# Kernel optimization log

Measured on AMD Instinct MI355X. Metric: run time of the kernel, lower is better.

The kernel has to match this reference:

```python
import jax, jax.numpy as jnp
import numpy as np

TEMP = 0.07
GAMMA1 = 0.8
GAMMA2 = 0.8
TAU = 0.1
BETA = 40.0
NUM_CT = 5
EPS = float(np.finfo(np.float32).eps)


def setup_inputs() -> dict:
    key = jax.random.key(0)
    ks = jax.random.split(key, 12)
    B, D, N, Bc = 8192, 512, 1000000, 4096
    img = jax.random.normal(ks[0], (B, D), jnp.float32)
    txt = jax.random.normal(ks[1], (B, D), jnp.float32)
    # CLIP-style unit-norm features keep sim in [-1,1] so exp() stays stable
    img = img / jnp.linalg.norm(img, axis=1, keepdims=True)
    txt = txt / jnp.linalg.norm(txt, axis=1, keepdims=True)
    image_ids = jax.random.randint(ks[2], (B,), 0, N)
    text_ids = jax.random.randint(ks[3], (B,), 0, N)
    slabel = jax.random.randint(ks[4], (B,), 0, 2)
    img_feas_c = jax.random.normal(ks[5], (Bc, D), jnp.float32)
    img_feas_c = img_feas_c / jnp.linalg.norm(img_feas_c, axis=1, keepdims=True)
    txt_feas_c = jax.random.normal(ks[6], (NUM_CT, D), jnp.float32)
    txt_feas_c = txt_feas_c / jnp.linalg.norm(txt_feas_c, axis=1, keepdims=True)
    labels_c = jax.random.randint(ks[7], (Bc,), 0, NUM_CT)
    last_loss_c = jax.random.uniform(ks[8], (Bc,), jnp.float32) * 2.0
    # persistent moving-average buffers (positive values, as they hold past exp-means)
    s_I = jax.random.uniform(ks[9], (N,), jnp.float32) + 0.5
    s_T = jax.random.uniform(ks[10], (N,), jnp.float32) + 0.5
    u = jnp.zeros((NUM_CT,), jnp.float32)
    return dict(image_features=img, text_features=txt, image_ids=image_ids,
                text_ids=text_ids, slabel=slabel, epoch=1,
                img_feas_c=img_feas_c, txt_feas_c=txt_feas_c, labels_c=labels_c,
                last_loss_c=last_loss_c, s_I=s_I, s_T=s_T, u=u)


def reference(image_features, text_features, image_ids, text_ids, slabel, epoch,
              img_feas_c, txt_feas_c, labels_c, last_loss_c, s_I, s_T, u):
    sg = jax.lax.stop_gradient
    # pairwise similarity GEMM  [B, B]
    sim = jnp.einsum('id,jd->ij', image_features, text_features)
    diag = jnp.diagonal(sim)
    pos = slabel == 1
    neg = ~pos
    pos_image_ids = image_ids[pos]
    pos_text_ids = text_ids[pos]
    # masked pairwise similarity differences: [P, B-P] and [B-P, P]
    image_diffs = (sim - diag[:, None])[pos][:, neg]
    text_diffs = (sim - diag[None, :])[neg][:, pos]
    image_diffs_d = sg(image_diffs / TEMP)
    text_diffs_d = sg(text_diffs / TEMP)
    exp_i = jnp.exp(image_diffs_d)
    exp_t = jnp.exp(text_diffs_d)
    g_I = jnp.mean(exp_i, axis=1, keepdims=True)   # [P, 1]
    g_T = jnp.mean(exp_t, axis=0, keepdims=True)   # [1, P]
    if epoch == 0:
        sI = g_I
        sT = g_T
    else:
        sI = ((1.0 - GAMMA1) * s_I[pos_image_ids] + GAMMA1 * g_I.squeeze()).reshape(g_I.shape)
        sT = ((1.0 - GAMMA1) * s_T[pos_text_ids] + GAMMA1 * g_T.squeeze()).reshape(g_T.shape)
    # persistent buffer scatter updates
    s_I_new = s_I.at[pos_image_ids].set(sI.squeeze())
    s_T_new = s_T.at[pos_text_ids].set(sT.squeeze())
    w_i = exp_i / (sI + EPS)
    w_t = exp_t / (sT + EPS)
    image_loss = jnp.mean(w_i * image_diffs, axis=1)
    text_loss = jnp.mean(w_t * text_diffs, axis=0)
    contrastive_loss = image_loss.mean() + text_loss.mean()
    # per-class CE penalty branch
    logits = (1.0 / TAU) * img_feas_c @ txt_feas_c.T           # [Bc, NUM_CT]
    logp = jax.nn.log_softmax(logits, axis=-1)
    ce = -logp[jnp.arange(logits.shape[0]), labels_c]          # [Bc]
    counts = jax.ops.segment_sum(jnp.ones_like(ce), labels_c, num_segments=NUM_CT)
    present = counts > 0
    safe_counts = jnp.maximum(counts, 1.0)
    mean_by_cls = jax.ops.segment_sum(ce, labels_c, num_segments=NUM_CT) / safe_counts
    mean_by_cls_last = jax.ops.segment_sum(last_loss_c, labels_c, num_segments=NUM_CT) / safe_counts
    cv = mean_by_cls - mean_by_cls_last
    u_sum = jnp.sum(jnp.where(present, u, 0.0))
    u_upd = jnp.where(u_sum == 0.0, sg(cv), (1.0 - GAMMA2) * u + GAMMA2 * sg(cv))
    u_new = jnp.where(present, u_upd, u)
    beta = BETA  # cosine=False
    cl = sg(jnp.maximum(beta * u_new, 0.0)) * mean_by_cls * TAU
    n_present = jnp.sum(present.astype(jnp.float32))
    constraint_mean = jnp.sum(jnp.where(present, cl, 0.0)) / n_present
    loss = contrastive_loss + constraint_mean
    return loss, s_I_new, s_T_new, u_new
```

## Files before the change

### kernel.cpp

```cpp
#include <hip/hip_runtime.h>

#define NBATCH 8192
#define DD 512
#define NIDS 1000000
#define BCNT 4096
#define NCT 5
#define INV_TEMP 14.285714285714286f
#define EPSF 1.1920929e-07f
#define FPSCALE 16.0f
#define INV_SIMSCALE (1.0f / 256.0f)

typedef __attribute__((ext_vector_type(4))) float f32x4;
typedef __attribute__((ext_vector_type(2))) long lx2;

#define OFF_LP     ((size_t)0)
#define OFF_CE1    ((size_t)1024)
#define OFF_CE2    ((size_t)2304)
#define OFF_CE3    ((size_t)3584)
#define OFF_POS    ((size_t)(32*1024))
#define OFF_RNK    ((size_t)(64*1024))
#define OFF_CNT    ((size_t)(96*1024))
#define OFF_DA     ((size_t)(100*1024))
#define OFF_RA0    ((size_t)(132*1024))
#define OFF_RB0    ((size_t)(164*1024))
#define OFF_RA1    ((size_t)(196*1024))
#define OFF_RB1    ((size_t)(228*1024))
#define OFF_SIV    ((size_t)(260*1024))
#define OFF_STV    ((size_t)(292*1024))
#define OFF_WINI   ((size_t)(324*1024))
#define OFF_WINT   (OFF_WINI + 4000000)
#define OFF_MA     (OFF_WINT + 4000000)
#define MATB       ((size_t)(8192*512*2))
#define OFF_MB     (OFF_MA + MATB)
#define OFF_MC     (OFF_MB + MATB)
#define OFF_MD     (OFF_MC + MATB)


__global__ __launch_bounds__(256) void k_pre(
        const float* __restrict__ sI, const float* __restrict__ sT,
        float* __restrict__ out,
        float* __restrict__ rA0, float* __restrict__ rB0,
        float* __restrict__ rA1, float* __restrict__ rB1,
        const int* __restrict__ slabel, int* __restrict__ pos,
        int* __restrict__ rnk, int* __restrict__ cnts,
        const float* __restrict__ imgc, const float* __restrict__ tfc,
        const int* __restrict__ labels, const float* __restrict__ lastl,
        float* __restrict__ ce1, float* __restrict__ ce2, float* __restrict__ ce3) {
    int bid = blockIdx.x;
    int tid = threadIdx.x;
    int iv = bid * 256 + tid;
    if (iv < NIDS) {
        out[1 + iv] = sI[iv];
        out[1 + NIDS + iv] = sT[iv];
    }
    if (iv < NBATCH) { rA0[iv] = 0.f; rB0[iv] = 0.f; rA1[iv] = 0.f; rB1[iv] = 0.f; }
    if (bid > 64) return;

    if (bid == 64) {
        __shared__ int sums[256];
        int base = tid * 32;
        int c = 0;
        for (int j = 0; j < 32; ++j) c += (slabel[base + j] == 1);
        sums[tid] = c;
        __syncthreads();
        for (int off = 1; off < 256; off <<= 1) {
            int add = (tid >= off) ? sums[tid - off] : 0;
            __syncthreads();
            sums[tid] += add;
            __syncthreads();
        }
        int p = sums[tid] - c;
        for (int j = 0; j < 32; ++j) {
            int idx = base + j;
            if (slabel[idx] == 1) { pos[p] = idx; rnk[idx] = p; p++; }
            else rnk[idx] = idx - p;
        }
        if (tid == 255) { cnts[0] = sums[255]; cnts[1] = NBATCH - sums[255]; }
    } else {
        int cb = bid;
        __shared__ float tS[NCT * DD];
        __shared__ float sce[NCT], scn[NCT], sls[NCT];
        for (int j = tid; j < NCT * DD; j += 256) tS[j] = tfc[j];
        if (tid < NCT) { sce[tid] = 0.f; scn[tid] = 0.f; sls[tid] = 0.f; }
        __syncthreads();
        int lane = tid & 63;
        int wid = tid >> 6;
        for (int it = 0; it < 16; ++it) {
            int r = it * 256 + cb * 4 + wid;
            const float4* ip = (const float4*)(imgc + (size_t)r * DD) + lane * 2;
            float4 a0 = ip[0], a1 = ip[1];
            float p[NCT];
#pragma unroll
            for (int c = 0; c < NCT; ++c) {
                const float* t = &tS[c * DD + lane * 8];
                p[c] = a0.x * t[0] + a0.y * t[1] + a0.z * t[2] + a0.w * t[3]
                     + a1.x * t[4] + a1.y * t[5] + a1.z * t[6] + a1.w * t[7];
            }
#pragma unroll
            for (int c = 0; c < NCT; ++c)
                for (int off = 32; off; off >>= 1) p[c] += __shfl_xor(p[c], off);
            if (lane == 0) {
                float l[NCT];
                float mx = -1e30f;
#pragma unroll
                for (int c = 0; c < NCT; ++c) { l[c] = p[c] * 10.0f; mx = fmaxf(mx, l[c]); }
                float ssum = 0.f;
#pragma unroll
                for (int c = 0; c < NCT; ++c) ssum += __expf(l[c] - mx);
                float lse = mx + __logf(ssum);
                int lb = labels[r];
                float ce = lse - l[lb];
                atomicAdd(&sce[lb], ce);
                atomicAdd(&scn[lb], 1.f);
                atomicAdd(&sls[lb], lastl[r]);
            }
        }
        __syncthreads();
        if (tid < NCT) {
            ce1[cb * 5 + tid] = sce[tid];
            ce2[cb * 5 + tid] = scn[tid];
            ce3[cb * 5 + tid] = sls[tid];
        }
    }
}

__global__ __launch_bounds__(256) void k_gather(
        const float* __restrict__ img, const float* __restrict__ txt,
        const int* __restrict__ slabel, const int* __restrict__ rnk,
        const int* __restrict__ image_ids, const int* __restrict__ text_ids,
        int* __restrict__ winI, int* __restrict__ winT,
        unsigned char* __restrict__ mA, unsigned char* __restrict__ mB,
        unsigned char* __restrict__ mC, unsigned char* __restrict__ mD,
        float* __restrict__ dA) {
    int tid = threadIdx.x;
    int kk = blockIdx.x * 256 + tid;
    if (kk < NBATCH) {
        winI[image_ids[kk]] = -1;
        winT[text_ids[kk]] = -1;
    }
    int i = blockIdx.x * 4 + (tid >> 6);
    int g = tid & 63;
    const float4* ip = (const float4*)(img + (size_t)i * DD) + g * 2;
    const float4* tp = (const float4*)(txt + (size_t)i * DD) + g * 2;
    float4 v0 = ip[0], v1 = ip[1], t0 = tp[0], t1 = tp[1];
    float part = v0.x * t0.x + v0.y * t0.y + v0.z * t0.z + v0.w * t0.w
               + v1.x * t1.x + v1.y * t1.y + v1.z * t1.z + v1.w * t1.w;
    for (int off = 32; off; off >>= 1) part += __shfl_xor(part, off);

    int lab = (slabel[i] == 1);
    int r = rnk[i];

    int ilo = __builtin_amdgcn_cvt_pk_fp8_f32(v0.x * FPSCALE, v0.y * FPSCALE, 0, 0);
    ilo = __builtin_amdgcn_cvt_pk_fp8_f32(v0.z * FPSCALE, v0.w * FPSCALE, ilo, 1);
    int ihi = __builtin_amdgcn_cvt_pk_fp8_f32(v1.x * FPSCALE, v1.y * FPSCALE, 0, 0);
    ihi = __builtin_amdgcn_cvt_pk_fp8_f32(v1.z * FPSCALE, v1.w * FPSCALE, ihi, 1);
    int tlo = __builtin_amdgcn_cvt_pk_fp8_f32(t0.x * FPSCALE, t0.y * FPSCALE, 0, 0);
    tlo = __builtin_amdgcn_cvt_pk_fp8_f32(t0.z * FPSCALE, t0.w * FPSCALE, tlo, 1);
    int thi = __builtin_amdgcn_cvt_pk_fp8_f32(t1.x * FPSCALE, t1.y * FPSCALE, 0, 0);
    thi = __builtin_amdgcn_cvt_pk_fp8_f32(t1.z * FPSCALE, t1.w * FPSCALE, thi, 1);

    int rl = r & 127;
    int cp = g & 7;
    int gran = cp & 3, half = cp >> 2;
    int swb = ((gran * 16) ^ ((rl & 6) << 3)) + half * 8;
    size_t off = (size_t)(r >> 7) * 65536 + (size_t)(g >> 3) * 8192 + rl * 64 + swb;
    unsigned char* dI = lab ? mA : mD;
    unsigned char* dT = lab ? mC : mB;
    *(int2*)(dI + off) = make_int2(ilo, ihi);
    *(int2*)(dT + off) = make_int2(tlo, thi);
    if (lab && g == 0) dA[r] = part;
}

__device__ __forceinline__ void gl16(const void* src, void* lds) {
    __builtin_amdgcn_global_load_lds((const __attribute__((address_space(1))) void*)src,
                                     (__attribute__((address_space(3))) void*)lds, 16, 0, 0);
}

#define VM4()  asm volatile("s_waitcnt vmcnt(4)" ::: "memory")
#define VM0()  asm volatile("s_waitcnt vmcnt(0)" ::: "memory")
#define BARR() asm volatile("s_barrier" ::: "memory")

__global__ __launch_bounds__(256) void k_gemm(
        const unsigned char* __restrict__ mA, const unsigned char* __restrict__ mB,
        const unsigned char* __restrict__ mC, const unsigned char* __restrict__ mD,
        const float* __restrict__ dA, const int* __restrict__ cnts,
        float* __restrict__ rA0, float* __restrict__ rB0,
        float* __restrict__ rA1, float* __restrict__ rB1) {
    int P = cnts[0], Nn = cnts[1];
    int bm = blockIdx.x * 128, bn = blockIdx.y * 128;
    if (bm >= P || bn >= Nn) return;
    int z = blockIdx.z;
    const unsigned char* Ap = (z ? mC : mA) + (size_t)blockIdx.x * 65536;
    const unsigned char* Bp = (z ? mD : mB) + (size_t)blockIdx.y * 65536;
    float* rA = z ? rA1 : rA0;
    float* rB = z ? rB1 : rB0;

    __shared__ __align__(16) char SRAW[36864];
    char* S = SRAW;

    int tid = threadIdx.x;
    int lane = tid & 63;
    int wid = tid >> 6;
    int wr = wid >> 1, wc = wid & 1;
    int bo = tid * 16;

    int kswz = ((lane >> 4) * 16) ^ ((lane & 6) << 3);
    int abyte = (wr * 64 + (lane & 15)) * 64 + kswz;
    int bbyte = (wc * 64 + (lane & 15)) * 64 + kswz;

    f32x4 acc[4][4];
#pragma unroll
    for (int m = 0; m < 4; ++m)
#pragma unroll
        for (int n = 0; n < 4; ++n) acc[m][n] = (f32x4){0.f, 0.f, 0.f, 0.f};

#define STAGE(kt, p) do { \
        gl16(Ap + (kt) * 8192 + bo,        S + (p) * 16384 + bo); \
        gl16(Ap + (kt) * 8192 + bo + 4096, S + (p) * 16384 + bo + 4096); \
        gl16(Bp + (kt) * 8192 + bo,        S + (p) * 16384 + 8192 + bo); \
        gl16(Bp + (kt) * 8192 + bo + 4096, S + (p) * 16384 + 8192 + bo + 4096); } while (0)

    STAGE(0, 0);
    STAGE(1, 1);
    VM4();
    BARR();

#pragma unroll
    for (int kt = 0; kt < 8; ++kt) {
        const int cur = kt & 1;
        const char* base = S + cur * 16384;
        lx2 af[4], bf[4];
#pragma unroll
        for (int m = 0; m < 4; ++m)
            af[m] = *(const lx2*)(base + abyte + m * 1024);
#pragma unroll
        for (int n = 0; n < 4; ++n)
            bf[n] = *(const lx2*)(base + 8192 + bbyte + n * 1024);
#pragma unroll
        for (int m = 0; m < 4; ++m)
#pragma unroll
            for (int n = 0; n < 4; ++n)
                acc[m][n] = __builtin_amdgcn_mfma_f32_16x16x32_fp8_fp8(af[m][0], bf[n][0], acc[m][n], 0, 0, 0);
#pragma unroll
        for (int m = 0; m < 4; ++m)
#pragma unroll
            for (int n = 0; n < 4; ++n)
                acc[m][n] = __builtin_amdgcn_mfma_f32_16x16x32_fp8_fp8(af[m][1], bf[n][1], acc[m][n], 0, 0, 0);
        if (kt < 7) {
            BARR();
            if (kt + 2 < 8) {
                STAGE(kt + 2, cur);
                VM4();
            } else {
                VM0();
            }
            BARR();
        }
    }
#undef STAGE

    BARR();
    float* F = (float*)SRAW;
    int col = lane & 15;
    int rsub = (lane >> 4) * 4;
    int rowbase = bm + wr * 64;
    int colb = bn + wc * 64 + col;
    int fb = ((wc << 7) + (wr << 6)) * 36 + col * 2;
#pragma unroll
    for (int m = 0; m < 4; ++m) {
#pragma unroll
        for (int r = 0; r < 4; ++r) {
            int wrow = m * 16 + rsub + r;
            float dv = dA[rowbase + wrow];
            float pa = 0.f, pb = 0.f;
#pragma unroll
            for (int n = 0; n < 4; ++n) {
                int gcol = colb + n * 16;
                float sv = acc[m][n][r] * INV_SIMSCALE;
                float df = sv - dv;
                float e = (gcol < Nn) ? __expf(df * INV_TEMP) : 0.f;
                pa += e;
                pb += e * df;
            }
            *(float2*)&F[fb + wrow * 36] = make_float2(pa, pb);
        }
    }
    BARR();
    {
        int row = tid >> 1;
        int half = tid & 1;
        const float4* Fr = (const float4*)&F[((half << 7) + row) * 36];
        float sa = 0.f, sb = 0.f;
#pragma unroll
        for (int q = 0; q < 8; ++q) {
            float4 v = Fr[q];
            sa += v.x + v.z;
            sb += v.y + v.w;
        }
        sa += __shfl_xor(sa, 1);
        sb += __shfl_xor(sb, 1);
        int grow = bm + row;
        if (!half && grow < P) {
            atomicAdd(&rA[grow], sa);
            atomicAdd(&rB[grow], sb);
        }
    }
}

__global__ void k_posfin(const int* __restrict__ cnts, const int* __restrict__ pos,
                         const float* __restrict__ rA0, const float* __restrict__ rB0,
                         const float* __restrict__ rA1, const float* __restrict__ rB1,
                         const int* __restrict__ image_ids, const int* __restrict__ text_ids,
                         const float* __restrict__ sIin, const float* __restrict__ sTin,
                         const int* __restrict__ epochp,
                         float* __restrict__ sIv, float* __restrict__ sTv,
                         int* __restrict__ winI, int* __restrict__ winT,
                         float* __restrict__ lp) {
    int k = blockIdx.x * 256 + threadIdx.x;
    int P = cnts[0], Nn = cnts[1];
    float invNn = 1.f / (float)Nn;
    int epoch = epochp[0];
    float lI = 0.f, lT = 0.f;
    if (k < P) {
        int i = pos[k];
        int idI = image_ids[i], idT = text_ids[i];
        float gI = rA0[k] * invNn;
        float sIvk = (epoch == 0) ? gI : 0.2f * sIin[idI] + 0.8f * gI;
        lI = (rB0[k] * invNn) / (sIvk + EPSF);
        float gT = rA1[k] * invNn;
        float sTvk = (epoch == 0) ? gT : 0.2f * sTin[idT] + 0.8f * gT;
        lT = (rB1[k] * invNn) / (sTvk + EPSF);
        sIv[k] = sIvk;
        sTv[k] = sTvk;
        atomicMax(&winI[idI], k);
        atomicMax(&winT[idT], k);
    }
    for (int off = 32; off; off >>= 1) { lI += __shfl_xor(lI, off); lT += __shfl_xor(lT, off); }
    if ((threadIdx.x & 63) == 0) {
        int slot = blockIdx.x * 4 + (threadIdx.x >> 6);
        lp[slot * 2] = lI;
        lp[slot * 2 + 1] = lT;
    }
}

__global__ void k_fin(const int* __restrict__ cnts, const int* __restrict__ pos,
                      const int* __restrict__ image_ids, const int* __restrict__ text_ids,
                      const int* __restrict__ winI, const int* __restrict__ winT,
                      const float* __restrict__ sIv, const float* __restrict__ sTv,
                      const float* __restrict__ lp, const float* __restrict__ ce1,
                      const float* __restrict__ ce2, const float* __restrict__ ce3,
                      const float* __restrict__ u, float* __restrict__ out) {
    int P = cnts[0];
    int k = blockIdx.x * 256 + threadIdx.x;
    if (k < P) {
        int i = pos[k];
        int a = image_ids[i];
        if (winI[a] == k) out[1 + a] = sIv[k];
        int b = text_ids[i];
        if (winT[b] == k) out[1 + NIDS + b] = sTv[k];
    }
    if (blockIdx.x == 0 && threadIdx.x < 64) {
        int lane = threadIdx.x;
        float lI = lp[2 * lane] + lp[2 * (lane + 64)];
        float lT = lp[2 * lane + 1] + lp[2 * (lane + 64) + 1];
        for (int off = 32; off; off >>= 1) { lI += __shfl_xor(lI, off); lT += __shfl_xor(lT, off); }
        float ce[NCT], cn[NCT], ls[NCT];
#pragma unroll
        for (int c = 0; c < NCT; ++c) {
            float a1 = ce1[lane * 5 + c], a2 = ce2[lane * 5 + c], a3 = ce3[lane * 5 + c];
            for (int off = 32; off; off >>= 1) {
                a1 += __shfl_xor(a1, off);
                a2 += __shfl_xor(a2, off);
                a3 += __shfl_xor(a3, off);
            }
            ce[c] = a1; cn[c] = a2; ls[c] = a3;
        }
        if (lane == 0) {
            float Pf = (float)P;
            float contrast = lI / Pf + lT / Pf;
            float u_sum = 0.f;
            float mc[NCT], cv[NCT], u_new[NCT];
            bool pres[NCT];
#pragma unroll
            for (int c = 0; c < NCT; ++c) {
                pres[c] = cn[c] > 0.f;
                float safe = fmaxf(cn[c], 1.f);
                mc[c] = ce[c] / safe;
                float ml = ls[c] / safe;
                cv[c] = mc[c] - ml;
                if (pres[c]) u_sum += u[c];
            }
            float np_ = 0.f, csum = 0.f;
#pragma unroll
            for (int c = 0; c < NCT; ++c) {
                float uu = (u_sum == 0.f) ? cv[c] : 0.2f * u[c] + 0.8f * cv[c];
                u_new[c] = pres[c] ? uu : u[c];
                if (pres[c]) {
                    np_ += 1.f;
                    csum += fmaxf(40.0f * u_new[c], 0.f) * mc[c] * 0.1f;
                }
                out[1 + 2 * NIDS + c] = u_new[c];
            }
            out[0] = contrast + csum / np_;
        }
    }
}

extern "C" void kernel_launch(void* const* d_in, const int* in_sizes, int n_in,
                              void* d_out, int out_size, void* d_ws, size_t ws_size,
                              hipStream_t stream) {
    const float* img = (const float*)d_in[0];
    const float* txt = (const float*)d_in[1];
    const int* image_ids = (const int*)d_in[2];
    const int* text_ids = (const int*)d_in[3];
    const int* slabel = (const int*)d_in[4];
    const int* epoch = (const int*)d_in[5];
    const float* imgc = (const float*)d_in[6];
    const float* tfc = (const float*)d_in[7];
    const int* labels = (const int*)d_in[8];
    const float* lastl = (const float*)d_in[9];
    const float* sI = (const float*)d_in[10];
    const float* sT = (const float*)d_in[11];
    const float* u = (const float*)d_in[12];
    float* out = (float*)d_out;
    char* ws = (char*)d_ws;

    float* lp = (float*)(ws + OFF_LP);
    float* ce1 = (float*)(ws + OFF_CE1);
    float* ce2 = (float*)(ws + OFF_CE2);
    float* ce3 = (float*)(ws + OFF_CE3);
    int* pos = (int*)(ws + OFF_POS);
    int* rnk = (int*)(ws + OFF_RNK);
    int* cnts = (int*)(ws + OFF_CNT);
    float* dA = (float*)(ws + OFF_DA);
    float* rA0 = (float*)(ws + OFF_RA0);
    float* rB0 = (float*)(ws + OFF_RB0);
    float* rA1 = (float*)(ws + OFF_RA1);
    float* rB1 = (float*)(ws + OFF_RB1);
    float* sIv = (float*)(ws + OFF_SIV);
    float* sTv = (float*)(ws + OFF_STV);
    int* winI = (int*)(ws + OFF_WINI);
    int* winT = (int*)(ws + OFF_WINT);
    unsigned char* mA = (unsigned char*)(ws + OFF_MA);
    unsigned char* mB = (unsigned char*)(ws + OFF_MB);
    unsigned char* mC = (unsigned char*)(ws + OFF_MC);
    unsigned char* mD = (unsigned char*)(ws + OFF_MD);

    k_pre<<<3972, 256, 0, stream>>>(sI, sT, out, rA0, rB0, rA1, rB1,
                                    slabel, pos, rnk, cnts,
                                    imgc, tfc, labels, lastl, ce1, ce2, ce3);
    k_gather<<<2048, 256, 0, stream>>>(img, txt, slabel, rnk, image_ids, text_ids,
                                       winI, winT, mA, mB, mC, mD, dA);
    k_gemm<<<dim3(64, 64, 2), 256, 0, stream>>>(mA, mB, mC, mD, dA, cnts, rA0, rB0, rA1, rB1);
    k_posfin<<<32, 256, 0, stream>>>(cnts, pos, rA0, rB0, rA1, rB1, image_ids, text_ids,
                                     sI, sT, epoch, sIv, sTv, winI, winT, lp);
    k_fin<<<32, 256, 0, stream>>>(cnts, pos, image_ids, text_ids, winI, winT,
                                  sIv, sTv, lp, ce1, ce2, ce3, u, out);
}
```

Before: 76.12 us.

## Split compaction into single-block kernel and merge copy/CE work into gather

The prefix-scan compaction of slabel moves into its own small one-block, 1024-thread kernel, which also zeroes the row accumulators. The large sI/sT copy into the output and the per-class CE blocks are folded into the gather kernel, which now launches 2112 blocks: each block copies two strided chunks, and the extra 64 blocks run the CE branch. This shortens the first launch, which gather waits on for rnk, and lets the memory-bound copy overlap with the fp8 packing work. In exchange there is an extra launch, and the gather blocks now carry more work and more register pressure.

```diff
diff --git a/kernel.cpp b/kernel.cpp
--- a/kernel.cpp
+++ b/kernel.cpp
@@ -36,48 +36,103 @@
 #define OFF_MD     (OFF_MC + MATB)
 
 
-__global__ __launch_bounds__(256) void k_pre(
+__global__ void k_compact(const int* __restrict__ slabel, int* __restrict__ pos,
+                          int* __restrict__ rnk, int* __restrict__ cnts,
+                          float* __restrict__ rA0, float* __restrict__ rB0,
+                          float* __restrict__ rA1, float* __restrict__ rB1) {
+    __shared__ int sums[1024];
+    int tid = threadIdx.x;
+#pragma unroll
+    for (int j = 0; j < 8; ++j) {
+        int v = tid * 8 + j;
+        rA0[v] = 0.f; rB0[v] = 0.f; rA1[v] = 0.f; rB1[v] = 0.f;
+    }
+    int flags[8];
+    int c = 0;
+    int base = tid * 8;
+#pragma unroll
+    for (int j = 0; j < 8; ++j) { flags[j] = (slabel[base + j] == 1); c += flags[j]; }
+    sums[tid] = c;
+    __syncthreads();
+    for (int off = 1; off < 1024; off <<= 1) {
+        int add = (tid >= off) ? sums[tid - off] : 0;
+        __syncthreads();
+        sums[tid] += add;
+        __syncthreads();
+    }
+    int p = sums[tid] - c;
+#pragma unroll
+    for (int j = 0; j < 8; ++j) {
+        int idx = base + j;
+        if (flags[j]) { pos[p] = idx; rnk[idx] = p; p++; }
+        else rnk[idx] = idx - p;
+    }
+    if (tid == 0) { cnts[0] = sums[1023]; cnts[1] = NBATCH - sums[1023]; }
+}
+
+__global__ __launch_bounds__(256) void k_gather(
+        const float* __restrict__ img, const float* __restrict__ txt,
+        const int* __restrict__ slabel, const int* __restrict__ rnk,
+        const int* __restrict__ image_ids, const int* __restrict__ text_ids,
+        int* __restrict__ winI, int* __restrict__ winT,
+        unsigned char* __restrict__ mA, unsigned char* __restrict__ mB,
+        unsigned char* __restrict__ mC, unsigned char* __restrict__ mD,
+        float* __restrict__ dA,
         const float* __restrict__ sI, const float* __restrict__ sT,
         float* __restrict__ out,
-        float* __restrict__ rA0, float* __restrict__ rB0,
-        float* __restrict__ rA1, float* __restrict__ rB1,
-        const int* __restrict__ slabel, int* __restrict__ pos,
-        int* __restrict__ rnk, int* __restrict__ cnts,
         const float* __restrict__ imgc, const float* __restrict__ tfc,
         const int* __restrict__ labels, const float* __restrict__ lastl,
         float* __restrict__ ce1, float* __restrict__ ce2, float* __restrict__ ce3) {
     int bid = blockIdx.x;
     int tid = threadIdx.x;
-    int iv = bid * 256 + tid;
-    if (iv < NIDS) {
-        out[1 + iv] = sI[iv];
-        out[1 + NIDS + iv] = sT[iv];
-    }
-    if (iv < NBATCH) { rA0[iv] = 0.f; rB0[iv] = 0.f; rA1[iv] = 0.f; rB1[iv] = 0.f; }
-    if (bid > 64) return;
-
-    if (bid == 64) {
-        __shared__ int sums[256];
-        int base = tid * 32;
-        int c = 0;
-        for (int j = 0; j < 32; ++j) c += (slabel[base + j] == 1);
-        sums[tid] = c;
-        __syncthreads();
-        for (int off = 1; off < 256; off <<= 1) {
-            int add = (tid >= off) ? sums[tid - off] : 0;
-            __syncthreads();
-            sums[tid] += add;
-            __syncthreads();
-        }
-        int p = sums[tid] - c;
-        for (int j = 0; j < 32; ++j) {
-            int idx = base + j;
-            if (slabel[idx] == 1) { pos[p] = idx; rnk[idx] = p; p++; }
-            else rnk[idx] = idx - p;
-        }
-        if (tid == 255) { cnts[0] = sums[255]; cnts[1] = NBATCH - sums[255]; }
+#pragma unroll
+    for (int rep = 0; rep < 2; ++rep) {
+        int iv = rep * 540672 + bid * 256 + tid;
+        if (iv < NIDS) {
+            out[1 + iv] = sI[iv];
+            out[1 + NIDS + iv] = sT[iv];
+        }
+    }
+
+    if (bid < 2048) {
+        int kk = bid * 256 + tid;
+        if (kk < NBATCH) {
+            winI[image_ids[kk]] = -1;
+            winT[text_ids[kk]] = -1;
+        }
+        int i = bid * 4 + (tid >> 6);
+        int g = tid & 63;
+        const float4* ip = (const float4*)(img + (size_t)i * DD) + g * 2;
+        const float4* tp = (const float4*)(txt + (size_t)i * DD) + g * 2;
+        float4 v0 = ip[0], v1 = ip[1], t0 = tp[0], t1 = tp[1];
+        float part = v0.x * t0.x + v0.y * t0.y + v0.z * t0.z + v0.w * t0.w
+                   + v1.x * t1.x + v1.y * t1.y + v1.z * t1.z + v1.w * t1.w;
+        for (int off = 32; off; off >>= 1) part += __shfl_xor(part, off);
+
+        int lab = (slabel[i] == 1);
+        int r = rnk[i];
+
+        int ilo = __builtin_amdgcn_cvt_pk_fp8_f32(v0.x * FPSCALE, v0.y * FPSCALE, 0, 0);
+        ilo = __builtin_amdgcn_cvt_pk_fp8_f32(v0.z * FPSCALE, v0.w * FPSCALE, ilo, 1);
+        int ihi = __builtin_amdgcn_cvt_pk_fp8_f32(v1.x * FPSCALE, v1.y * FPSCALE, 0, 0);
+        ihi = __builtin_amdgcn_cvt_pk_fp8_f32(v1.z * FPSCALE, v1.w * FPSCALE, ihi, 1);
+        int tlo = __builtin_amdgcn_cvt_pk_fp8_f32(t0.x * FPSCALE, t0.y * FPSCALE, 0, 0);
+        tlo = __builtin_amdgcn_cvt_pk_fp8_f32(t0.z * FPSCALE, t0.w * FPSCALE, tlo, 1);
+        int thi = __builtin_amdgcn_cvt_pk_fp8_f32(t1.x * FPSCALE, t1.y * FPSCALE, 0, 0);
+        thi = __builtin_amdgcn_cvt_pk_fp8_f32(t1.z * FPSCALE, t1.w * FPSCALE, thi, 1);
+
+        int rl = r & 127;
+        int cp = g & 7;
+        int gran = cp & 3, half = cp >> 2;
+        int swb = ((gran * 16) ^ ((rl & 6) << 3)) + half * 8;
+        size_t off = (size_t)(r >> 7) * 65536 + (size_t)(g >> 3) * 8192 + rl * 64 + swb;
+        unsigned char* dI = lab ? mA : mD;
+        unsigned char* dT = lab ? mC : mB;
+        *(int2*)(dI + off) = make_int2(ilo, ihi);
+        *(int2*)(dT + off) = make_int2(tlo, thi);
+        if (lab && g == 0) dA[r] = part;
     } else {
-        int cb = bid;
+        int cb = bid - 2048;
         __shared__ float tS[NCT * DD];
         __shared__ float sce[NCT], scn[NCT], sls[NCT];
         for (int j = tid; j < NCT * DD; j += 256) tS[j] = tfc[j];
@@ -122,53 +177,6 @@
             ce3[cb * 5 + tid] = sls[tid];
         }
     }
-}
-
-__global__ __launch_bounds__(256) void k_gather(
-        const float* __restrict__ img, const float* __restrict__ txt,
-        const int* __restrict__ slabel, const int* __restrict__ rnk,
-        const int* __restrict__ image_ids, const int* __restrict__ text_ids,
-        int* __restrict__ winI, int* __restrict__ winT,
-        unsigned char* __restrict__ mA, unsigned char* __restrict__ mB,
-        unsigned char* __restrict__ mC, unsigned char* __restrict__ mD,
-        float* __restrict__ dA) {
-    int tid = threadIdx.x;
-    int kk = blockIdx.x * 256 + tid;
-    if (kk < NBATCH) {
-        winI[image_ids[kk]] = -1;
-        winT[text_ids[kk]] = -1;
-    }
-    int i = blockIdx.x * 4 + (tid >> 6);
-    int g = tid & 63;
-    const float4* ip = (const float4*)(img + (size_t)i * DD) + g * 2;
-    const float4* tp = (const float4*)(txt + (size_t)i * DD) + g * 2;
-    float4 v0 = ip[0], v1 = ip[1], t0 = tp[0], t1 = tp[1];
-    float part = v0.x * t0.x + v0.y * t0.y + v0.z * t0.z + v0.w * t0.w
-               + v1.x * t1.x + v1.y * t1.y + v1.z * t1.z + v1.w * t1.w;
-    for (int off = 32; off; off >>= 1) part += __shfl_xor(part, off);
-
-    int lab = (slabel[i] == 1);
-    int r = rnk[i];
-
-    int ilo = __builtin_amdgcn_cvt_pk_fp8_f32(v0.x * FPSCALE, v0.y * FPSCALE, 0, 0);
-    ilo = __builtin_amdgcn_cvt_pk_fp8_f32(v0.z * FPSCALE, v0.w * FPSCALE, ilo, 1);
-    int ihi = __builtin_amdgcn_cvt_pk_fp8_f32(v1.x * FPSCALE, v1.y * FPSCALE, 0, 0);
-    ihi = __builtin_amdgcn_cvt_pk_fp8_f32(v1.z * FPSCALE, v1.w * FPSCALE, ihi, 1);
-    int tlo = __builtin_amdgcn_cvt_pk_fp8_f32(t0.x * FPSCALE, t0.y * FPSCALE, 0, 0);
-    tlo = __builtin_amdgcn_cvt_pk_fp8_f32(t0.z * FPSCALE, t0.w * FPSCALE, tlo, 1);
-    int thi = __builtin_amdgcn_cvt_pk_fp8_f32(t1.x * FPSCALE, t1.y * FPSCALE, 0, 0);
-    thi = __builtin_amdgcn_cvt_pk_fp8_f32(t1.z * FPSCALE, t1.w * FPSCALE, thi, 1);
-
-    int rl = r & 127;
-    int cp = g & 7;
-    int gran = cp & 3, half = cp >> 2;
-    int swb = ((gran * 16) ^ ((rl & 6) << 3)) + half * 8;
-    size_t off = (size_t)(r >> 7) * 65536 + (size_t)(g >> 3) * 8192 + rl * 64 + swb;
-    unsigned char* dI = lab ? mA : mD;
-    unsigned char* dT = lab ? mC : mB;
-    *(int2*)(dI + off) = make_int2(ilo, ihi);
-    *(int2*)(dT + off) = make_int2(tlo, thi);
-    if (lab && g == 0) dA[r] = part;
 }
 
 __device__ __forceinline__ void gl16(const void* src, void* lds) {
@@ -446,11 +454,11 @@
     unsigned char* mC = (unsigned char*)(ws + OFF_MC);
     unsigned char* mD = (unsigned char*)(ws + OFF_MD);
 
-    k_pre<<<3972, 256, 0, stream>>>(sI, sT, out, rA0, rB0, rA1, rB1,
-                                    slabel, pos, rnk, cnts,
-                                    imgc, tfc, labels, lastl, ce1, ce2, ce3);
-    k_gather<<<2048, 256, 0, stream>>>(img, txt, slabel, rnk, image_ids, text_ids,
-                                       winI, winT, mA, mB, mC, mD, dA);
+    k_compact<<<1, 1024, 0, stream>>>(slabel, pos, rnk, cnts, rA0, rB0, rA1, rB1);
+    k_gather<<<2112, 256, 0, stream>>>(img, txt, slabel, rnk, image_ids, text_ids,
+                                       winI, winT, mA, mB, mC, mD, dA,
+                                       sI, sT, out, imgc, tfc, labels, lastl,
+                                       ce1, ce2, ce3);
     k_gemm<<<dim3(64, 64, 2), 256, 0, stream>>>(mA, mB, mC, mD, dA, cnts, rA0, rB0, rA1, rB1);
     k_posfin<<<32, 256, 0, stream>>>(cnts, pos, rA0, rB0, rA1, rB1, image_ids, text_ids,
                                      sI, sT, epoch, sIv, sTv, winI, winT, lp);
```

After: 84.61 us. 11.2% more time.
